# Performance work log

Hardware: AMD Instinct MI355X
Metric: run time of the kernel (lower is better)

The kernel has to match this reference:

```python
import jax, jax.numpy as jnp
import numpy as np

B, N, D = 8, 2048, 256
BIG = 1e9  # max_int_value used to mask the diagonal
LN_EPS = 1e-5  # F.layer_norm default eps


def setup_inputs() -> dict:
    key = jax.random.key(0)
    kq, kk = jax.random.split(key)
    q = jax.random.normal(kq, (B, N, D), dtype=jnp.float32)
    k = jax.random.normal(kk, (B, N, D), dtype=jnp.float32)
    return {"q": q, "k": k, "top_k_instances": 100, "top_k_relationships": 5}


def _forward(q, k, K, R):
    b, n, d = q.shape
    # dense QK^T + softmax over keys -> (b, n, n)
    scores1 = jax.nn.softmax(jnp.einsum('bid,bjd->bij', q, k), axis=-1)
    # instance selection: top-K of the softmaxed diagonal, sorted ascending
    diag = jnp.diagonal(scores1, axis1=-2, axis2=-1)           # (b, n)
    top_idx = jnp.sort(jax.lax.top_k(diag, K)[1], axis=-1)      # (b, K)
    # gather selected rows then selected columns -> (b, K, K)
    sel = jnp.take_along_axis(scores1, top_idx[:, :, None], axis=1)   # (b, K, n)
    rel = jnp.take_along_axis(sel, jnp.broadcast_to(top_idx[:, None, :], (b, K, K)), axis=2)
    # mask diagonal with BIG (masked_fill_ with eye)
    rel = jnp.where(jnp.eye(K, dtype=bool)[None], BIG, rel)
    # top-R relationships per selected instance; torch recovers them via
    # scatter(-1)+where, which yields row-major order with ascending column
    # indices inside each row -> equivalent to sorting top-k indices per row.
    rel_idx = jnp.sort(jax.lax.top_k(rel, R)[1], axis=-1)       # (b, K, R)
    rows = jnp.broadcast_to(jnp.arange(K)[:, None], (K, R)).reshape(-1)  # (K*R,)
    subj = top_idx[:, rows]                                     # (b, K*R) original subject ids
    obj = jnp.take_along_axis(top_idx, rel_idx.reshape(b, K * R), axis=-1)  # (b, K*R)
    batch_ids = jnp.broadcast_to(jnp.arange(b)[:, None], (b, K * R))
    soi = jnp.stack([batch_ids, subj, obj], axis=-1)            # (b, K*R, 3)
    # gather embeddings from q and layer-norm (no affine)
    se = jnp.take_along_axis(q, subj[:, :, None], axis=1)       # (b, K*R, d)
    oe = jnp.take_along_axis(q, obj[:, :, None], axis=1)
    re = se + oe
    mu = jnp.mean(re, axis=-1, keepdims=True)
    var = jnp.var(re, axis=-1, keepdims=True)
    re = (re - mu) * jax.lax.rsqrt(var + LN_EPS)
    return scores1, soi, re


def reference(q, k, top_k_instances, top_k_relationships):
    return _forward(q, k, top_k_instances, top_k_relationships)
```

## Files before the change

### kernel.cpp

```cpp
#include <hip/hip_runtime.h>
#include <math.h>

#define BB 8
#define NN 2048
#define DD 256
#define KK 100
#define RR 5
#define BIGV 1000000000.0f
#define LN_EPS 1e-5f

typedef __attribute__((ext_vector_type(8))) short short8;
typedef __attribute__((ext_vector_type(4))) float floatx4;

__device__ static inline unsigned short f2bf_rne(float x) {
  unsigned int u = __float_as_uint(x);
  unsigned int r = (u + 0x7FFFu + ((u >> 16) & 1u)) >> 16;
  return (unsigned short)r;
}
__device__ static inline float bf2f(unsigned short h) {
  return __uint_as_float(((unsigned int)h) << 16);
}

__device__ static inline void gl_lds16(const unsigned short* g, unsigned short* l) {
  __builtin_amdgcn_global_load_lds(
      (const __attribute__((address_space(1))) unsigned int*)(g),
      (__attribute__((address_space(3))) unsigned int*)(l), 16, 0, 0);
}

__global__ __launch_bounds__(256) void split_bf16(const float* __restrict__ q,
                                                  const float* __restrict__ k,
                                                  ushort4* __restrict__ qhi,
                                                  ushort4* __restrict__ qlo,
                                                  ushort4* __restrict__ khi,
                                                  ushort4* __restrict__ klo) {
  const int n4 = BB * NN * DD / 4;
  const float4* src = (blockIdx.y == 0) ? (const float4*)q : (const float4*)k;
  ushort4* hi = blockIdx.y ? khi : qhi;
  ushort4* lo = blockIdx.y ? klo : qlo;
  for (int i = blockIdx.x * 256 + threadIdx.x; i < n4; i += gridDim.x * 256) {
    float4 v = src[i];
    ushort4 h, l;
    h.x = f2bf_rne(v.x); l.x = f2bf_rne(v.x - bf2f(h.x));
    h.y = f2bf_rne(v.y); l.y = f2bf_rne(v.y - bf2f(h.y));
    h.z = f2bf_rne(v.z); l.z = f2bf_rne(v.z - bf2f(h.z));
    h.w = f2bf_rne(v.w); l.w = f2bf_rne(v.w - bf2f(h.w));
    hi[i] = h; lo[i] = l;
  }
}

__global__ __launch_bounds__(256) void gemm_mfma_split(
    const unsigned short* __restrict__ qhi, const unsigned short* __restrict__ qlo,
    const unsigned short* __restrict__ khi, const unsigned short* __restrict__ klo,
    float* __restrict__ s) {
  __shared__ unsigned short lds[4][8][512];
  const int b = blockIdx.z;
  const int i0 = blockIdx.y * 128, j0 = blockIdx.x * 128;
  const int t = threadIdx.x;
  const int w = t >> 6, L = t & 63;
  const int wx = w & 1, wy = w >> 1;
  const int q_ = L >> 4, m_ = L & 15;

  const size_t bofs = (size_t)b * NN * DD;
  const unsigned short* base;
  {
    const unsigned short* bases0 = qhi + bofs;
    const unsigned short* bases1 = qlo + bofs;
    const unsigned short* bases2 = khi + bofs;
    const unsigned short* bases3 = klo + bofs;
    base = (w == 0) ? bases0 : (w == 1) ? bases1 : (w == 2) ? bases2 : bases3;
  }
  const int rowbase = (w < 2 ? i0 : j0);

  floatx4 acc[4][4];
#pragma unroll
  for (int i = 0; i < 4; ++i)
#pragma unroll
    for (int j = 0; j < 4; ++j) acc[i][j] = (floatx4){0.f, 0.f, 0.f, 0.f};

  for (int kb0 = 0; kb0 < DD; kb0 += 32) {
#pragma unroll
    for (int r = 0; r < 8; ++r) {
      const unsigned short* gp =
          base + (size_t)(rowbase + r * 16 + m_) * DD + kb0 + q_ * 8;
      gl_lds16(gp, &lds[w][r][0]);
    }
    __syncthreads();

    short8 ah[4], al[4], bh[4], bl[4];
#pragma unroll
    for (int i = 0; i < 4; ++i) {
      ah[i] = *(const short8*)&lds[0][wy * 4 + i][L * 8];
      al[i] = *(const short8*)&lds[1][wy * 4 + i][L * 8];
      bh[i] = *(const short8*)&lds[2][wx * 4 + i][L * 8];
      bl[i] = *(const short8*)&lds[3][wx * 4 + i][L * 8];
    }
#pragma unroll
    for (int i = 0; i < 4; ++i)
#pragma unroll
      for (int j = 0; j < 4; ++j) {
        acc[i][j] = __builtin_amdgcn_mfma_f32_16x16x32_bf16(ah[i], bh[j], acc[i][j], 0, 0, 0);
        acc[i][j] = __builtin_amdgcn_mfma_f32_16x16x32_bf16(ah[i], bl[j], acc[i][j], 0, 0, 0);
        acc[i][j] = __builtin_amdgcn_mfma_f32_16x16x32_bf16(al[i], bh[j], acc[i][j], 0, 0, 0);
      }
    __syncthreads();
  }

#pragma unroll
  for (int i = 0; i < 4; ++i)
#pragma unroll
    for (int j = 0; j < 4; ++j)
#pragma unroll
      for (int r = 0; r < 4; ++r) {
        int row = i0 + wy * 64 + i * 16 + q_ * 4 + r;
        int col = j0 + wx * 64 + j * 16 + m_;
        s[((size_t)b * NN + row) * NN + col] = acc[i][j][r];
      }
}

__global__ __launch_bounds__(256) void gemm_logits(const float* __restrict__ q,
                                                   const float* __restrict__ k,
                                                   float* __restrict__ s) {
  __shared__ float As[32][132];
  __shared__ float Bs[32][132];
  const int b = blockIdx.z;
  const int i0 = blockIdx.y * 128;
  const int j0 = blockIdx.x * 128;
  const int t = threadIdx.x;
  const int tx = t & 15;
  const int ty = t >> 4;
  const float* qb = q + (size_t)b * NN * DD;
  const float* kb = k + (size_t)b * NN * DD;

  float acc[8][8];
#pragma unroll
  for (int i = 0; i < 8; ++i)
#pragma unroll
    for (int j = 0; j < 8; ++j) acc[i][j] = 0.f;

  for (int kb0 = 0; kb0 < DD; kb0 += 32) {
#pragma unroll
    for (int l = 0; l < 4; ++l) {
      int f = l * 256 + t;
      int row = f >> 3;
      int c4 = (f & 7) * 4;
      float4 va = *(const float4*)(qb + (size_t)(i0 + row) * DD + kb0 + c4);
      float4 vb = *(const float4*)(kb + (size_t)(j0 + row) * DD + kb0 + c4);
      As[c4 + 0][row] = va.x; As[c4 + 1][row] = va.y;
      As[c4 + 2][row] = va.z; As[c4 + 3][row] = va.w;
      Bs[c4 + 0][row] = vb.x; Bs[c4 + 1][row] = vb.y;
      Bs[c4 + 2][row] = vb.z; Bs[c4 + 3][row] = vb.w;
    }
    __syncthreads();
#pragma unroll
    for (int kk = 0; kk < 32; ++kk) {
      float a[8], bv[8];
      *(float4*)&a[0] = *(const float4*)&As[kk][ty * 8];
      *(float4*)&a[4] = *(const float4*)&As[kk][ty * 8 + 4];
      *(float4*)&bv[0] = *(const float4*)&Bs[kk][tx * 8];
      *(float4*)&bv[4] = *(const float4*)&Bs[kk][tx * 8 + 4];
#pragma unroll
      for (int i = 0; i < 8; ++i)
#pragma unroll
        for (int j = 0; j < 8; ++j) acc[i][j] += a[i] * bv[j];
    }
    __syncthreads();
  }

#pragma unroll
  for (int i = 0; i < 8; ++i) {
    size_t row = (size_t)(i0 + ty * 8 + i);
    float* po = s + ((size_t)b * NN + row) * NN + j0 + tx * 8;
    *(float4*)po = make_float4(acc[i][0], acc[i][1], acc[i][2], acc[i][3]);
    *(float4*)(po + 4) = make_float4(acc[i][4], acc[i][5], acc[i][6], acc[i][7]);
  }
}

__device__ inline float pick4(float4 v, int j) {
  return j == 0 ? v.x : (j == 1 ? v.y : (j == 2 ? v.z : v.w));
}

__global__ __launch_bounds__(256) void softmax_rows(float* __restrict__ s,
                                                    float* __restrict__ diag) {
  const int bi = blockIdx.x;
  const int irow = bi & (NN - 1);
  const int t = threadIdx.x;
  float4* rowp = (float4*)(s + (size_t)bi * NN);
  float4 v0 = rowp[t];
  float4 v1 = rowp[256 + t];

  __shared__ float red[4];
  float m = fmaxf(fmaxf(fmaxf(v0.x, v0.y), fmaxf(v0.z, v0.w)),
                  fmaxf(fmaxf(v1.x, v1.y), fmaxf(v1.z, v1.w)));
#pragma unroll
  for (int off = 32; off; off >>= 1) m = fmaxf(m, __shfl_xor(m, off));
  if ((t & 63) == 0) red[t >> 6] = m;
  __syncthreads();
  m = fmaxf(fmaxf(red[0], red[1]), fmaxf(red[2], red[3]));
  __syncthreads();

  float4 e0, e1;
  e0.x = expf(v0.x - m); e0.y = expf(v0.y - m);
  e0.z = expf(v0.z - m); e0.w = expf(v0.w - m);
  e1.x = expf(v1.x - m); e1.y = expf(v1.y - m);
  e1.z = expf(v1.z - m); e1.w = expf(v1.w - m);
  float sum = e0.x + e0.y + e0.z + e0.w + e1.x + e1.y + e1.z + e1.w;
#pragma unroll
  for (int off = 32; off; off >>= 1) sum += __shfl_xor(sum, off);
  if ((t & 63) == 0) red[t >> 6] = sum;
  __syncthreads();
  sum = red[0] + red[1] + red[2] + red[3];

  float inv = 1.0f / sum;
  float4 s0 = make_float4(e0.x * inv, e0.y * inv, e0.z * inv, e0.w * inv);
  float4 s1 = make_float4(e1.x * inv, e1.y * inv, e1.z * inv, e1.w * inv);
  rowp[t] = s0;
  rowp[256 + t] = s1;

  int c0 = t * 4;
  if (irow >= c0 && irow < c0 + 4) diag[bi] = pick4(s0, irow - c0);
  int c1 = 1024 + t * 4;
  if (irow >= c1 && irow < c1 + 4) diag[bi] = pick4(s1, irow - c1);
}

__global__ __launch_bounds__(1024) void topk_diag(const float* __restrict__ diag,
                                                  int* __restrict__ topidx) {
  const int b = blockIdx.x;
  const int t = threadIdx.x;
  __shared__ unsigned long long key[NN];
  __shared__ int idxs[KK];

#pragma unroll
  for (int sIt = 0; sIt < 2; ++sIt) {
    int i = t + sIt * 1024;
    unsigned int vb = __float_as_uint(diag[b * NN + i]);
    key[i] = ((unsigned long long)vb << 32) | (unsigned int)(NN - 1 - i);
  }
  __syncthreads();

  for (int kstep = 2; kstep <= NN; kstep <<= 1) {
    for (int j = kstep >> 1; j > 0; j >>= 1) {
      int i = ((t & ~(j - 1)) << 1) | (t & (j - 1));
      int l = i | j;
      unsigned long long a = key[i];
      unsigned long long c = key[l];
      bool desc = ((i & kstep) == 0);
      if (desc ? (a < c) : (a > c)) { key[i] = c; key[l] = a; }
      __syncthreads();
    }
  }

  if (t < KK) idxs[t] = NN - 1 - (int)(unsigned int)(key[t] & 0xFFFFFFFFu);
  __syncthreads();
  if (t < KK) {
    int myidx = idxs[t];
    int rank = 0;
#pragma unroll 4
    for (int j = 0; j < KK; ++j) rank += (idxs[j] < myidx) ? 1 : 0;
    topidx[b * KK + rank] = myidx;
  }
}

__global__ __launch_bounds__(256) void rel_topk(const float* __restrict__ s,
                                                const int* __restrict__ topidx,
                                                float* __restrict__ soi,
                                                int2* __restrict__ pairs) {
  const int b = blockIdx.x;
  const int t = threadIdx.x;
  __shared__ int tix[KK];
  __shared__ float rel[KK][KK + 1];
  if (t < KK) tix[t] = topidx[b * KK + t];
  __syncthreads();

  for (int e = t; e < KK * KK; e += 256) {
    int i = e / KK;
    int j = e - i * KK;
    rel[i][j] = (i == j) ? BIGV : s[((size_t)b * NN + tix[i]) * NN + tix[j]];
  }
  __syncthreads();

  if (t < KK) {
    int sel[RR];
#pragma unroll
    for (int r = 0; r < RR; ++r) sel[r] = -1;
#pragma unroll
    for (int r = 0; r < RR; ++r) {
      float best = -2.f;
      int bj = -1;
      for (int j = 0; j < KK; ++j) {
        bool taken = false;
#pragma unroll
        for (int sN = 0; sN < RR; ++sN)
          if (sN < r && sel[sN] == j) taken = true;
        if (taken) continue;
        float v = rel[t][j];
        if (v > best) { best = v; bj = j; }
      }
      sel[r] = bj;
    }
#pragma unroll
    for (int a2 = 0; a2 < RR; ++a2)
#pragma unroll
      for (int b2 = a2 + 1; b2 < RR; ++b2)
        if (sel[b2] < sel[a2]) { int tmp = sel[a2]; sel[a2] = sel[b2]; sel[b2] = tmp; }

    int subj = tix[t];
#pragma unroll
    for (int r = 0; r < RR; ++r) {
      int obj = tix[sel[r]];
      size_t p = ((size_t)b * KK + t) * RR + r;
      soi[p * 3 + 0] = (float)b;
      soi[p * 3 + 1] = (float)subj;
      soi[p * 3 + 2] = (float)obj;
      pairs[p] = make_int2(subj, obj);
    }
  }
}

__global__ __launch_bounds__(64) void edge_ln(const float* __restrict__ q,
                                              const int2* __restrict__ pairs,
                                              float* __restrict__ re) {
  const int p = blockIdx.x;
  const int b = p / (KK * RR);
  const int l = threadIdx.x;
  int2 pr = pairs[p];
  const float4* qs = (const float4*)(q + ((size_t)b * NN + pr.x) * DD);
  const float4* qo = (const float4*)(q + ((size_t)b * NN + pr.y) * DD);
  float4 a = qs[l];
  float4 o = qo[l];
  a.x += o.x; a.y += o.y; a.z += o.z; a.w += o.w;
  float sum = a.x + a.y + a.z + a.w;
  float sq = a.x * a.x + a.y * a.y + a.z * a.z + a.w * a.w;
#pragma unroll
  for (int off = 32; off; off >>= 1) {
    sum += __shfl_xor(sum, off);
    sq += __shfl_xor(sq, off);
  }
  float mu = sum * (1.f / DD);
  float var = sq * (1.f / DD) - mu * mu;
  float rs = rsqrtf(var + LN_EPS);
  float4 r4 = make_float4((a.x - mu) * rs, (a.y - mu) * rs,
                          (a.z - mu) * rs, (a.w - mu) * rs);
  ((float4*)(re + (size_t)p * DD))[l] = r4;
}

extern "C" void kernel_launch(void* const* d_in, const int* in_sizes, int n_in,
                              void* d_out, int out_size, void* d_ws, size_t ws_size,
                              hipStream_t stream) {
  const float* q = (const float*)d_in[0];
  const float* k = (const float*)d_in[1];

  float* out = (float*)d_out;
  float* scores = out;
  float* soi = out + (size_t)BB * NN * NN;
  float* re = soi + (size_t)BB * KK * RR * 3;

  char* ws = (char*)d_ws;
  float* diag = (float*)ws;
  int* topidx = (int*)(ws + (size_t)BB * NN * 4);
  int2* pairs = (int2*)(ws + (size_t)BB * NN * 4 + (size_t)BB * KK * 4);
  const size_t small_end = 128 * 1024;
  const size_t plane = (size_t)BB * NN * DD * 2;
  const bool use_mfma = ws_size >= small_end + 4 * plane;

  if (use_mfma) {
    unsigned short* qhi = (unsigned short*)(ws + small_end);
    unsigned short* qlo = (unsigned short*)(ws + small_end + plane);
    unsigned short* khi = (unsigned short*)(ws + small_end + 2 * plane);
    unsigned short* klo = (unsigned short*)(ws + small_end + 3 * plane);
    split_bf16<<<dim3(1024, 2), 256, 0, stream>>>(q, k, (ushort4*)qhi, (ushort4*)qlo,
                                                  (ushort4*)khi, (ushort4*)klo);
    gemm_mfma_split<<<dim3(NN / 128, NN / 128, BB), 256, 0, stream>>>(qhi, qlo, khi, klo,
                                                                      scores);
  } else {
    gemm_logits<<<dim3(NN / 128, NN / 128, BB), 256, 0, stream>>>(q, k, scores);
  }
  softmax_rows<<<dim3(BB * NN), 256, 0, stream>>>(scores, diag);
  topk_diag<<<dim3(BB), 1024, 0, stream>>>(diag, topidx);
  rel_topk<<<dim3(BB), 256, 0, stream>>>(scores, topidx, soi, pairs);
  edge_ln<<<dim3(BB * KK * RR), 64, 0, stream>>>(q, pairs, re);
}
```

Baseline: 326.1 us.

## Double-buffer MFMA GEMM loads, swizzle block order, parallelize relationship top-k

The split-bf16 MFMA GEMM now double-buffers its LDS tiles. The next k-slice is issued via global_load_lds before the current slice is computed, and explicit vmcnt waits plus raw barriers replace __syncthreads, so loads can overlap compute. Block indices are remapped so neighbouring blocks spread across batches, which changes cache and channel locality. The rel_topk kernel goes from 8 blocks of 256 threads to 800 single-wave blocks, each finding one row's top-5 with packed 64-bit keys and wave shuffle reductions instead of serial scans. Doubled LDS use may cut occupancy, and the hand-written waitcnt counts must match the number of loads in flight.

```diff
diff --git a/kernel.cpp b/kernel.cpp
--- a/kernel.cpp
+++ b/kernel.cpp
@@ -52,9 +52,15 @@
     const unsigned short* __restrict__ qhi, const unsigned short* __restrict__ qlo,
     const unsigned short* __restrict__ khi, const unsigned short* __restrict__ klo,
     float* __restrict__ s) {
-  __shared__ unsigned short lds[4][8][512];
-  const int b = blockIdx.z;
-  const int i0 = blockIdx.y * 128, j0 = blockIdx.x * 128;
+  __shared__ unsigned short lds[2][4][8][512];
+
+  const int lid = blockIdx.x + ((blockIdx.y + (blockIdx.z << 4)) << 4);
+  const int swz = ((lid & 7) << 8) + (lid >> 3);
+  const int bx = swz & 15;
+  const int by = (swz >> 4) & 15;
+  const int b = swz >> 8;
+  const int i0 = by * 128, j0 = bx * 128;
+
   const int t = threadIdx.x;
   const int w = t >> 6, L = t & 63;
   const int wx = w & 1, wy = w >> 1;
@@ -63,13 +69,14 @@
   const size_t bofs = (size_t)b * NN * DD;
   const unsigned short* base;
   {
-    const unsigned short* bases0 = qhi + bofs;
-    const unsigned short* bases1 = qlo + bofs;
-    const unsigned short* bases2 = khi + bofs;
-    const unsigned short* bases3 = klo + bofs;
-    base = (w == 0) ? bases0 : (w == 1) ? bases1 : (w == 2) ? bases2 : bases3;
+    const unsigned short* b0 = qhi + bofs;
+    const unsigned short* b1 = qlo + bofs;
+    const unsigned short* b2 = khi + bofs;
+    const unsigned short* b3 = klo + bofs;
+    base = (w == 0) ? b0 : (w == 1) ? b1 : (w == 2) ? b2 : b3;
   }
   const int rowbase = (w < 2 ? i0 : j0);
+  const unsigned short* gbase = base + (size_t)(rowbase + m_) * DD + q_ * 8;
 
   floatx4 acc[4][4];
 #pragma unroll
@@ -77,22 +84,29 @@
 #pragma unroll
     for (int j = 0; j < 4; ++j) acc[i][j] = (floatx4){0.f, 0.f, 0.f, 0.f};
 
-  for (int kb0 = 0; kb0 < DD; kb0 += 32) {
-#pragma unroll
-    for (int r = 0; r < 8; ++r) {
-      const unsigned short* gp =
-          base + (size_t)(rowbase + r * 16 + m_) * DD + kb0 + q_ * 8;
-      gl_lds16(gp, &lds[w][r][0]);
-    }
-    __syncthreads();
+#define STAGE(buf, kb0)                                              \
+  _Pragma("unroll") for (int r = 0; r < 8; ++r)                      \
+      gl_lds16(gbase + (size_t)r * 16 * DD + (kb0), &lds[buf][w][r][0]);
+
+  STAGE(0, 0);
+  int cur = 0;
+#pragma unroll
+  for (int it = 0; it < 8; ++it) {
+    if (it < 7) {
+      STAGE(cur ^ 1, (it + 1) * 32);
+      asm volatile("s_waitcnt vmcnt(8)" ::: "memory");
+    } else {
+      asm volatile("s_waitcnt vmcnt(0)" ::: "memory");
+    }
+    __builtin_amdgcn_s_barrier();
 
     short8 ah[4], al[4], bh[4], bl[4];
 #pragma unroll
     for (int i = 0; i < 4; ++i) {
-      ah[i] = *(const short8*)&lds[0][wy * 4 + i][L * 8];
-      al[i] = *(const short8*)&lds[1][wy * 4 + i][L * 8];
-      bh[i] = *(const short8*)&lds[2][wx * 4 + i][L * 8];
-      bl[i] = *(const short8*)&lds[3][wx * 4 + i][L * 8];
+      ah[i] = *(const short8*)&lds[cur][0][wy * 4 + i][L * 8];
+      al[i] = *(const short8*)&lds[cur][1][wy * 4 + i][L * 8];
+      bh[i] = *(const short8*)&lds[cur][2][wx * 4 + i][L * 8];
+      bl[i] = *(const short8*)&lds[cur][3][wx * 4 + i][L * 8];
     }
 #pragma unroll
     for (int i = 0; i < 4; ++i)
@@ -102,8 +116,10 @@
         acc[i][j] = __builtin_amdgcn_mfma_f32_16x16x32_bf16(ah[i], bl[j], acc[i][j], 0, 0, 0);
         acc[i][j] = __builtin_amdgcn_mfma_f32_16x16x32_bf16(al[i], bh[j], acc[i][j], 0, 0, 0);
       }
-    __syncthreads();
-  }
+    __builtin_amdgcn_s_barrier();
+    cur ^= 1;
+  }
+#undef STAGE
 
 #pragma unroll
   for (int i = 0; i < 4; ++i)
@@ -260,54 +276,54 @@
   }
 }
 
-__global__ __launch_bounds__(256) void rel_topk(const float* __restrict__ s,
-                                                const int* __restrict__ topidx,
-                                                float* __restrict__ soi,
-                                                int2* __restrict__ pairs) {
-  const int b = blockIdx.x;
-  const int t = threadIdx.x;
-  __shared__ int tix[KK];
-  __shared__ float rel[KK][KK + 1];
-  if (t < KK) tix[t] = topidx[b * KK + t];
-  __syncthreads();
-
-  for (int e = t; e < KK * KK; e += 256) {
-    int i = e / KK;
-    int j = e - i * KK;
-    rel[i][j] = (i == j) ? BIGV : s[((size_t)b * NN + tix[i]) * NN + tix[j]];
-  }
-  __syncthreads();
-
-  if (t < KK) {
-    int sel[RR];
-#pragma unroll
-    for (int r = 0; r < RR; ++r) sel[r] = -1;
-#pragma unroll
-    for (int r = 0; r < RR; ++r) {
-      float best = -2.f;
-      int bj = -1;
-      for (int j = 0; j < KK; ++j) {
-        bool taken = false;
-#pragma unroll
-        for (int sN = 0; sN < RR; ++sN)
-          if (sN < r && sel[sN] == j) taken = true;
-        if (taken) continue;
-        float v = rel[t][j];
-        if (v > best) { best = v; bj = j; }
-      }
-      sel[r] = bj;
-    }
+__global__ __launch_bounds__(64) void rel_topk(const float* __restrict__ s,
+                                               const int* __restrict__ topidx,
+                                               float* __restrict__ soi,
+                                               int2* __restrict__ pairs) {
+  const int b = blockIdx.y;
+  const int i = blockIdx.x;
+  const int l = threadIdx.x;
+  const int* tixb = topidx + b * KK;
+  const int subj = tixb[i];
+  const float* srow = s + ((size_t)b * NN + subj) * NN;
+
+  const int j0 = l, j1 = l + 64;
+  int c0 = tixb[j0];
+  float v0 = (j0 == i) ? BIGV : srow[c0];
+  unsigned long long k0 =
+      ((unsigned long long)__float_as_uint(v0) << 32) | (unsigned int)(KK - 1 - j0);
+  unsigned long long k1 = 0ull;
+  if (j1 < KK) {
+    int c1 = tixb[j1];
+    float v1 = (j1 == i) ? BIGV : srow[c1];
+    k1 = ((unsigned long long)__float_as_uint(v1) << 32) | (unsigned int)(KK - 1 - j1);
+  }
+
+  int sel[RR];
+#pragma unroll
+  for (int r = 0; r < RR; ++r) {
+    unsigned long long best = k0 > k1 ? k0 : k1;
+#pragma unroll
+    for (int off = 32; off; off >>= 1) {
+      unsigned long long o = __shfl_xor(best, off);
+      if (o > best) best = o;
+    }
+    int js = KK - 1 - (int)(unsigned int)(best & 0xFFFFFFFFull);
+    sel[r] = js;
+    if (j0 == js) k0 = 0ull;
+    if (j1 == js) k1 = 0ull;
+  }
+
+  if (l == 0) {
 #pragma unroll
     for (int a2 = 0; a2 < RR; ++a2)
 #pragma unroll
       for (int b2 = a2 + 1; b2 < RR; ++b2)
         if (sel[b2] < sel[a2]) { int tmp = sel[a2]; sel[a2] = sel[b2]; sel[b2] = tmp; }
-
-    int subj = tix[t];
 #pragma unroll
     for (int r = 0; r < RR; ++r) {
-      int obj = tix[sel[r]];
-      size_t p = ((size_t)b * KK + t) * RR + r;
+      int obj = tixb[sel[r]];
+      size_t p = ((size_t)b * KK + i) * RR + r;
       soi[p * 3 + 0] = (float)b;
       soi[p * 3 + 1] = (float)subj;
       soi[p * 3 + 2] = (float)obj;
@@ -376,6 +392,6 @@
   }
   softmax_rows<<<dim3(BB * NN), 256, 0, stream>>>(scores, diag);
   topk_diag<<<dim3(BB), 1024, 0, stream>>>(diag, topidx);
-  rel_topk<<<dim3(BB), 256, 0, stream>>>(scores, topidx, soi, pairs);
+  rel_topk<<<dim3(KK, BB), 64, 0, stream>>>(scores, topidx, soi, pairs);
   edge_ln<<<dim3(BB * KK * RR), 64, 0, stream>>>(q, pairs, re);
 }
```

New measurement: 281.7 us. 13.6% less time.
